# Kernel optimization log

Measured on AMD Instinct MI355X. Metric: run time of the kernel, lower is better.

## Reference

```python
import jax, jax.numpy as jnp
import numpy as np

B, S, L, V = 512, 17, 81, 13030
ENC, OE, PE, H = 240, 80, 60, 200
IN = ENC + OE + PE  # 380
TEMPERATURE = 1.0


def setup_inputs() -> dict:
    key = jax.random.key(0)
    ks = jax.random.split(key, 16)
    enc = jax.random.normal(ks[0], (B, L, ENC), dtype=jnp.float32)
    in_adj_phase = jnp.zeros((B,), dtype=bool)
    loc_idxs = jax.random.randint(ks[1], (B, L), 0, S)  # which step each location decodes at
    order_masks = jax.random.bernoulli(ks[2], 0.2, (B, S, V))
    power_1h = jnp.eye(7, dtype=jnp.float32)[jax.random.randint(ks[3], (B,), 0, 7)]
    w = 0.1
    return {
        'enc': enc,
        'in_adj_phase': in_adj_phase,
        'loc_idxs': loc_idxs,
        'order_masks': order_masks,
        'power_1h': power_1h,
        'order_embedding': w * jax.random.normal(ks[4], (V, OE), dtype=jnp.float32),
        'power_W': w * jax.random.normal(ks[5], (PE, 7), dtype=jnp.float32),
        'power_b': w * jax.random.normal(ks[6], (PE,), dtype=jnp.float32),
        'W_ih': w * jax.random.normal(ks[7], (4 * H, IN), dtype=jnp.float32),
        'W_hh': w * jax.random.normal(ks[8], (4 * H, H), dtype=jnp.float32),
        'b_ih': w * jax.random.normal(ks[9], (4 * H,), dtype=jnp.float32),
        'b_hh': w * jax.random.normal(ks[10], (4 * H,), dtype=jnp.float32),
        'out_W': w * jax.random.normal(ks[11], (V, H), dtype=jnp.float32),
        'out_b': w * jax.random.normal(ks[12], (V,), dtype=jnp.float32),
        'master_alignments': jax.random.uniform(ks[13], (L, L), dtype=jnp.float32),
    }


def reference(enc, in_adj_phase, loc_idxs, order_masks, power_1h,
              order_embedding, power_W, power_b, W_ih, W_hh, b_ih, b_hh,
              out_W, out_b, master_alignments):
    # eval mode: dropout masks are not applied (self.training is False)
    power_emb = power_1h @ power_W.T + power_b  # [B, PE]
    invalid = ~jnp.any(loc_idxs != -1, axis=1)  # [B] rows with no orders to give
    keys = jax.random.split(jax.random.key(42), S)

    def step_fn(carry, xs):
        h, c, order_emb = carry
        step, mask_t, k = xs  # mask_t: [B, V]
        # alignment over locations decoded at this step
        sel = ((loc_idxs == step) | (loc_idxs == -2)).astype(enc.dtype)  # [B, L]
        align = sel @ master_alignments  # [B, L]
        denom = jnp.sum(align, axis=1, keepdims=True)
        align = jnp.where(denom != 0, align / denom, 0.0)  # NaN -> 0 as in torch
        loc_enc = jnp.einsum('bl,bld->bd', align, enc)  # [B, ENC]
        x = jnp.concatenate([loc_enc, order_emb, power_emb], axis=1)  # [B, IN]
        gates = x @ W_ih.T + b_ih + h @ W_hh.T + b_hh  # torch gate order i,f,g,o
        i, f, g, o = jnp.split(gates, 4, axis=1)
        c_new = jax.nn.sigmoid(f) * c + jax.nn.sigmoid(i) * jnp.tanh(g)
        h_new = jax.nn.sigmoid(o) * jnp.tanh(c_new)
        scores = h_new @ out_W.T + out_b  # [B, V]
        m = jnp.where(invalid[:, None], True, mask_t)
        scores = jnp.minimum(scores, m.astype(scores.dtype) * 1e9 - 1e8)
        idx = jax.random.categorical(k, scores / TEMPERATURE, axis=-1)  # [B]
        order_emb_new = order_embedding[idx]  # [B, OE]
        return (h_new, c_new, order_emb_new), (idx, scores)

    carry0 = (jnp.zeros((B, H), enc.dtype), jnp.zeros((B, H), enc.dtype),
              jnp.zeros((B, OE), enc.dtype))
    xs = (jnp.arange(S), jnp.transpose(order_masks, (1, 0, 2)), keys)
    _, (idxs, scores) = jax.lax.scan(step_fn, carry0, xs)
    return jnp.transpose(idxs, (1, 0)), jnp.transpose(scores, (1, 0, 2))
```

## Files before the change

kernel.cpp:

```cpp
#include <hip/hip_runtime.h>
#include <math.h>

#define NB 512
#define NS 17
#define NL 81
#define NV 13030
#define NENC 240
#define NOE 80
#define NPE 60
#define NH 200
#define NIN 380
#define NG 800
#define KP 224
#define KG 608
#define NVP 13056
#define NGP 832
#define NBLK 204

#define XH_ENC 224
#define XH_OE  464
#define XH_PE  544

typedef short bf8_t __attribute__((ext_vector_type(8)));
typedef float f4_t __attribute__((ext_vector_type(4)));

__device__ __forceinline__ unsigned short f2bf(float f) {
  unsigned u = __float_as_uint(f);
  unsigned r = (u + 0x7fffu + ((u >> 16) & 1u)) >> 16;
  return (unsigned short)r;
}

__device__ __host__ __forceinline__ unsigned rotl32h(unsigned x, int d) {
  return (x << d) | (x >> (32 - d));
}
__device__ __host__ __forceinline__ void threefry2x32(
    unsigned k0, unsigned k1, unsigned x0, unsigned x1,
    unsigned& y0, unsigned& y1) {
  unsigned ks2 = k0 ^ k1 ^ 0x1BD11BDAu;
  x0 += k0; x1 += k1;
#define TFR(r) { x0 += x1; x1 = rotl32h(x1, r); x1 ^= x0; }
  TFR(13) TFR(15) TFR(26) TFR(6)
  x0 += k1;  x1 += ks2 + 1u;
  TFR(17) TFR(29) TFR(16) TFR(24)
  x0 += ks2; x1 += k0 + 2u;
  TFR(13) TFR(15) TFR(26) TFR(6)
  x0 += k0;  x1 += k1 + 3u;
  TFR(17) TFR(29) TFR(16) TFR(24)
  x0 += k1;  x1 += ks2 + 4u;
  TFR(13) TFR(15) TFR(26) TFR(6)
  x0 += ks2; x1 += k0 + 5u;
#undef TFR
  y0 = x0; y1 = x1;
}

__device__ __forceinline__ float gumbel_from_bits(unsigned bits) {
  float u = __uint_as_float((bits >> 9) | 0x3f800000u) - 1.0f;
  if (u == 0.0f) u = 1.17549435e-38f;
  return -__logf(-__logf(u));
}

__global__ void __launch_bounds__(256) prep_wcat_kernel(
    const float* __restrict__ W_ih, const float* __restrict__ W_hh,
    unsigned short* __restrict__ Wcat) {
  int t = blockIdx.x * 256 + threadIdx.x;
  if (t >= NGP * KG) return;
  int n = t / KG, k = t % KG;
  float v = 0.f;
  if (n < NG) {
    if (k < NH) v = W_hh[n * NH + k];
    else if (k >= XH_ENC && k < XH_PE + NPE) v = W_ih[n * NIN + (k - XH_ENC)];
  }
  Wcat[t] = f2bf(v);
}

__global__ void __launch_bounds__(256) prep_outw_kernel(
    const float* __restrict__ out_W, unsigned short* __restrict__ outWb) {
  int t = blockIdx.x * 256 + threadIdx.x;
  if (t >= NVP * KP) return;
  int n = t / KP, k = t % KP;
  outWb[t] = f2bf((n < NV && k < NH) ? out_W[n * NH + k] : 0.f);
}

__global__ void __launch_bounds__(256) misc_kernel(
    const float* __restrict__ power_1h, const float* __restrict__ power_W,
    const float* __restrict__ power_b, const int* __restrict__ loc_idxs,
    const float* __restrict__ b_ih, const float* __restrict__ b_hh,
    unsigned short* __restrict__ xh, float* __restrict__ bcat,
    int* __restrict__ invalid) {
  int t = blockIdx.x * 256 + threadIdx.x;
  if (t < NB * NPE) {
    int b = t / NPE, p = t % NPE;
    float a = power_b[p];
#pragma unroll
    for (int k = 0; k < 7; ++k) a = fmaf(power_1h[b * 7 + k], power_W[p * 7 + k], a);
    xh[(size_t)b * KG + XH_PE + p] = f2bf(a);
  }
  if (t < NG) bcat[t] = b_ih[t] + b_hh[t];
  if (t < NB) {
    bool any = false;
    for (int l = 0; l < NL; ++l) any = any || (loc_idxs[t * NL + l] != -1);
    invalid[t] = any ? 0 : 1;
  }
}

__global__ void __launch_bounds__(256) build_x_kernel(
    const int* __restrict__ loc_idxs, const float* __restrict__ MA,
    const float* __restrict__ enc, unsigned short* __restrict__ xh, int step) {
  __shared__ float sel[NL];
  __shared__ float aln[NL];
  __shared__ float denom;
  const int b = blockIdx.x, tid = threadIdx.x;
  if (tid < NL) {
    int li = loc_idxs[b * NL + tid];
    sel[tid] = (li == step || li == -2) ? 1.0f : 0.0f;
  }
  __syncthreads();
  if (tid < NL) {
    float a = 0.f;
    for (int l = 0; l < NL; ++l) a = fmaf(sel[l], MA[l * NL + tid], a);
    aln[tid] = a;
  }
  __syncthreads();
  if (tid == 0) {
    float d = 0.f;
    for (int l = 0; l < NL; ++l) d += aln[l];
    denom = d;
  }
  __syncthreads();
  if (tid < NL) aln[tid] = (denom != 0.f) ? aln[tid] / denom : 0.0f;
  __syncthreads();
  if (tid < NENC) {
    const float* eb = enc + (size_t)b * NL * NENC + tid;
    float a = 0.f;
    for (int l = 0; l < NL; ++l) a = fmaf(aln[l], eb[(size_t)l * NENC], a);
    xh[(size_t)b * KG + XH_ENC + tid] = f2bf(a);
  }
}

__device__ __forceinline__ void mfma_nt_16x64(
    const unsigned short* __restrict__ A, const unsigned short* __restrict__ B,
    int lda, int ldb, int m0w, int n0, int nk, f4_t acc[4]) {
  const int lane = threadIdx.x & 63;
  const int tx = lane & 15, quad = lane >> 4;
  const unsigned short* ap = A + (size_t)(m0w + tx) * lda + quad * 8;
  const unsigned short* bp0 = B + (size_t)(n0 + tx) * ldb + quad * 8;
  for (int kc = 0; kc < nk; ++kc) {
    bf8_t a = *(const bf8_t*)(ap + kc * 32);
#pragma unroll
    for (int jf = 0; jf < 4; ++jf) {
      bf8_t b = *(const bf8_t*)(bp0 + (size_t)jf * 16 * ldb + kc * 32);
      acc[jf] = __builtin_amdgcn_mfma_f32_16x16x32_bf16(a, b, acc[jf], 0, 0, 0);
    }
  }
}

__global__ void __launch_bounds__(256) gates_kernel(
    const unsigned short* __restrict__ xh, const unsigned short* __restrict__ Wcat,
    const float* __restrict__ bcat, float* __restrict__ gates) {
  const int w = threadIdx.x >> 6;
  const int lane = threadIdx.x & 63;
  const int tx = lane & 15, quad = lane >> 4;
  const int m0w = blockIdx.y * 64 + w * 16;
  const int n0 = blockIdx.x * 64;
  f4_t acc[4] = {};
  mfma_nt_16x64(xh, Wcat, KG, KG, m0w, n0, KG / 32, acc);
#pragma unroll
  for (int jf = 0; jf < 4; ++jf) {
    int n = n0 + jf * 16 + tx;
    if (n >= NG) continue;
    float bias = bcat[n];
#pragma unroll
    for (int reg = 0; reg < 4; ++reg) {
      int m = m0w + quad * 4 + reg;
      gates[(size_t)m * NG + n] = acc[jf][reg] + bias;
    }
  }
}

__global__ void __launch_bounds__(256) lstm_cell_kernel(
    const float* __restrict__ gates, unsigned short* __restrict__ xh,
    float* __restrict__ c) {
  int t = blockIdx.x * 256 + threadIdx.x;
  if (t >= NB * NH) return;
  int b = t / NH, j = t % NH;
  const float* g = gates + (size_t)b * NG;
  float gi = g[j], gf = g[NH + j], gg = g[2 * NH + j], go = g[3 * NH + j];
  float si = 1.f / (1.f + expf(-gi));
  float sf = 1.f / (1.f + expf(-gf));
  float so = 1.f / (1.f + expf(-go));
  float cn = sf * c[t] + si * tanhf(gg);
  float hn = so * tanhf(cn);
  c[t] = cn;
  xh[(size_t)b * KG + j] = f2bf(hn);
}

__global__ void __launch_bounds__(256) scores_kernel(
    const unsigned short* __restrict__ xh, const unsigned short* __restrict__ outWb,
    const float* __restrict__ out_b, const int* __restrict__ order_masks,
    const int* __restrict__ invalid, float* __restrict__ out,
    float* __restrict__ pval, int* __restrict__ pidx,
    int step, unsigned k0, unsigned k1) {
  const int w = threadIdx.x >> 6;
  const int lane = threadIdx.x & 63;
  const int tx = lane & 15, quad = lane >> 4;
  const int m0w = blockIdx.y * 64 + w * 16;
  const int n0 = blockIdx.x * 64;
  f4_t acc[4] = {};
  mfma_nt_16x64(xh, outWb, KG, KP, m0w, n0, KP / 32, acc);

  float bias[4];
  int nn[4];
#pragma unroll
  for (int jf = 0; jf < 4; ++jf) {
    nn[jf] = n0 + jf * 16 + tx;
    bias[jf] = (nn[jf] < NV) ? out_b[nn[jf]] : 0.f;
  }

  float bval[4];
  int bidx[4];
#pragma unroll
  for (int reg = 0; reg < 4; ++reg) {
    const int m = m0w + quad * 4 + reg;
    const int inv = invalid[m];
    const int* mrow = order_masks + (size_t)m * NS * NV + (size_t)step * NV;
    float* orow = out + (size_t)NB * NS + ((size_t)m * NS + step) * (size_t)NV;
    float vals[4];
#pragma unroll
    for (int jf = 0; jf < 4; ++jf) {
      int n = nn[jf];
      float v = -1.0e8f;
      if (n < NV) {
        int msk = inv ? 1 : mrow[n];
        v = fminf(acc[jf][reg] + bias[jf], msk ? 9.0e8f : -1.0e8f);
        orow[n] = v;
      }
      vals[jf] = v;
    }
    unsigned base = (unsigned)m * (unsigned)NV;
    unsigned y0, y1, y2, y3;
    threefry2x32(k0, k1, base + (unsigned)nn[0], base + (unsigned)nn[1], y0, y1);
    threefry2x32(k0, k1, base + (unsigned)nn[2], base + (unsigned)nn[3], y2, y3);
    float g[4] = {gumbel_from_bits(y0), gumbel_from_bits(y1),
                  gumbel_from_bits(y2), gumbel_from_bits(y3)};
    float bv = -INFINITY; int bi = 0;
#pragma unroll
    for (int jf = 0; jf < 4; ++jf) {
      float cnd = (nn[jf] < NV) ? vals[jf] + g[jf] : -INFINITY;
      if (cnd > bv) { bv = cnd; bi = nn[jf]; }
    }
    bval[reg] = bv; bidx[reg] = bi;
  }
#pragma unroll
  for (int s = 8; s >= 1; s >>= 1) {
#pragma unroll
    for (int reg = 0; reg < 4; ++reg) {
      float ov = __shfl_xor(bval[reg], s);
      int oi = __shfl_xor(bidx[reg], s);
      if (ov > bval[reg]) { bval[reg] = ov; bidx[reg] = oi; }
    }
  }
#pragma unroll
  for (int reg = 0; reg < 4; ++reg) {
    if (tx == reg) {
      int m = m0w + quad * 4 + reg;
      pval[(size_t)m * NBLK + blockIdx.x] = bval[reg];
      pidx[(size_t)m * NBLK + blockIdx.x] = bidx[reg];
    }
  }
}

__global__ void __launch_bounds__(256) sample_kernel(
    const float* __restrict__ pval, const int* __restrict__ pidx,
    const float* __restrict__ order_embedding, unsigned short* __restrict__ xh,
    float* __restrict__ out, int step) {
  const int m = blockIdx.x, tid = threadIdx.x;
  __shared__ float sv[256];
  __shared__ int si[256];
  float v = -INFINITY; int i = 0;
  if (tid < NBLK) { v = pval[(size_t)m * NBLK + tid]; i = pidx[(size_t)m * NBLK + tid]; }
  sv[tid] = v; si[tid] = i;
  __syncthreads();
  for (int off = 128; off > 0; off >>= 1) {
    if (tid < off) {
      float v2 = sv[tid + off]; int i2 = si[tid + off];
      if (v2 > sv[tid] || (v2 == sv[tid] && i2 < si[tid])) { sv[tid] = v2; si[tid] = i2; }
    }
    __syncthreads();
  }
  if (tid == 0) out[m * NS + step] = (float)si[0];
  if (tid < NOE) {
    int idx = si[0];
    xh[(size_t)m * KG + XH_OE + tid] = f2bf(order_embedding[(size_t)idx * NOE + tid]);
  }
}

extern "C" void kernel_launch(void* const* d_in, const int* in_sizes, int n_in,
                              void* d_out, int out_size, void* d_ws, size_t ws_size,
                              hipStream_t stream) {
  const float* enc          = (const float*)d_in[0];
  const int*   loc_idxs     = (const int*)d_in[2];
  const int*   order_masks  = (const int*)d_in[3];
  const float* power_1h     = (const float*)d_in[4];
  const float* order_embedding = (const float*)d_in[5];
  const float* power_W      = (const float*)d_in[6];
  const float* power_b      = (const float*)d_in[7];
  const float* W_ih         = (const float*)d_in[8];
  const float* W_hh         = (const float*)d_in[9];
  const float* b_ih         = (const float*)d_in[10];
  const float* b_hh         = (const float*)d_in[11];
  const float* out_W        = (const float*)d_in[12];
  const float* out_b        = (const float*)d_in[13];
  const float* MA           = (const float*)d_in[14];

  float* ws      = (float*)d_ws;
  float* c       = ws;
  float* gates   = c + NB * NH;
  float* pval    = gates + NB * NG;
  float* bcat    = pval + NB * NBLK;
  int*   pidx    = (int*)(bcat + NG);
  int*   invalid = pidx + NB * NBLK;
  unsigned short* xh    = (unsigned short*)(invalid + NB);
  unsigned short* Wcat  = xh + (size_t)NB * KG;
  unsigned short* outWb = Wcat + (size_t)NGP * KG;

  float* out = (float*)d_out;

  hipMemsetAsync(xh, 0, sizeof(unsigned short) * (size_t)NB * KG, stream);
  hipMemsetAsync(c, 0, sizeof(float) * (size_t)NB * NH, stream);
  misc_kernel<<<(NB * NPE + 255) / 256, 256, 0, stream>>>(
      power_1h, power_W, power_b, loc_idxs, b_ih, b_hh, xh, bcat, invalid);
  prep_wcat_kernel<<<(NGP * KG + 255) / 256, 256, 0, stream>>>(W_ih, W_hh, Wcat);
  prep_outw_kernel<<<(NVP * KP + 255) / 256, 256, 0, stream>>>(out_W, outWb);

  unsigned key[2 * NS];
  for (unsigned i = 0; i < NS; ++i) {
    unsigned y0, y1;
    threefry2x32(0u, 42u, i, i + NS, y0, y1);
    key[2 * i] = y0;
    threefry2x32(0u, 42u, i, i + NS, y0, y1);
    key[2 * i + 1] = y1;
  }

  dim3 gGates(NGP / 64, NB / 64);
  dim3 gScores(NBLK, NB / 64);
  for (int s = 0; s < NS; ++s) {
    build_x_kernel<<<NB, 256, 0, stream>>>(loc_idxs, MA, enc, xh, s);
    gates_kernel<<<gGates, 256, 0, stream>>>(xh, Wcat, bcat, gates);
    lstm_cell_kernel<<<(NB * NH + 255) / 256, 256, 0, stream>>>(gates, xh, c);
    scores_kernel<<<gScores, 256, 0, stream>>>(
        xh, outWb, out_b, order_masks, invalid, out, pval, pidx,
        s, key[2 * s], key[2 * s + 1]);
    sample_kernel<<<NB, 256, 0, stream>>>(pval, pidx, order_embedding, xh, out, s);
  }
}
```

Before: 1.942 ms.

## Hoist input projections out of LSTM loop and fuse gates, cell and sampling

The parts of the input-gate projection that do not depend on the recurrence are precomputed once before the loop. These are the location-encoding contribution for every step, the power embedding plus bias, and a table of order-embedding gate contributions over the whole vocabulary. Each step then only does the h·W_hh GEMM, fused with the LSTM cell, the previous step's argmax reduction and a table lookup. This cuts per-step launches and GEMM width, in exchange for larger precomputed buffers. The precomputed gate terms are stored in bf16, which adds rounding, and the argmax tie-break is made deterministic.

```diff
diff --git a/kernel.cpp b/kernel.cpp
--- a/kernel.cpp
+++ b/kernel.cpp
@@ -12,14 +12,12 @@
 #define NIN 380
 #define NG 800
 #define KP 224
-#define KG 608
+#define KE 256
+#define KO 96
 #define NVP 13056
 #define NGP 832
 #define NBLK 204
-
-#define XH_ENC 224
-#define XH_OE  464
-#define XH_PE  544
+#define LDG 840
 
 typedef short bf8_t __attribute__((ext_vector_type(8)));
 typedef float f4_t __attribute__((ext_vector_type(4)));
@@ -28,6 +26,9 @@
   unsigned u = __float_as_uint(f);
   unsigned r = (u + 0x7fffu + ((u >> 16) & 1u)) >> 16;
   return (unsigned short)r;
+}
+__device__ __forceinline__ float bf2f(unsigned short u) {
+  return __uint_as_float((unsigned)u << 16);
 }
 
 __device__ __host__ __forceinline__ unsigned rotl32h(unsigned x, int d) {
@@ -59,84 +60,6 @@
   return -__logf(-__logf(u));
 }
 
-__global__ void __launch_bounds__(256) prep_wcat_kernel(
-    const float* __restrict__ W_ih, const float* __restrict__ W_hh,
-    unsigned short* __restrict__ Wcat) {
-  int t = blockIdx.x * 256 + threadIdx.x;
-  if (t >= NGP * KG) return;
-  int n = t / KG, k = t % KG;
-  float v = 0.f;
-  if (n < NG) {
-    if (k < NH) v = W_hh[n * NH + k];
-    else if (k >= XH_ENC && k < XH_PE + NPE) v = W_ih[n * NIN + (k - XH_ENC)];
-  }
-  Wcat[t] = f2bf(v);
-}
-
-__global__ void __launch_bounds__(256) prep_outw_kernel(
-    const float* __restrict__ out_W, unsigned short* __restrict__ outWb) {
-  int t = blockIdx.x * 256 + threadIdx.x;
-  if (t >= NVP * KP) return;
-  int n = t / KP, k = t % KP;
-  outWb[t] = f2bf((n < NV && k < NH) ? out_W[n * NH + k] : 0.f);
-}
-
-__global__ void __launch_bounds__(256) misc_kernel(
-    const float* __restrict__ power_1h, const float* __restrict__ power_W,
-    const float* __restrict__ power_b, const int* __restrict__ loc_idxs,
-    const float* __restrict__ b_ih, const float* __restrict__ b_hh,
-    unsigned short* __restrict__ xh, float* __restrict__ bcat,
-    int* __restrict__ invalid) {
-  int t = blockIdx.x * 256 + threadIdx.x;
-  if (t < NB * NPE) {
-    int b = t / NPE, p = t % NPE;
-    float a = power_b[p];
-#pragma unroll
-    for (int k = 0; k < 7; ++k) a = fmaf(power_1h[b * 7 + k], power_W[p * 7 + k], a);
-    xh[(size_t)b * KG + XH_PE + p] = f2bf(a);
-  }
-  if (t < NG) bcat[t] = b_ih[t] + b_hh[t];
-  if (t < NB) {
-    bool any = false;
-    for (int l = 0; l < NL; ++l) any = any || (loc_idxs[t * NL + l] != -1);
-    invalid[t] = any ? 0 : 1;
-  }
-}
-
-__global__ void __launch_bounds__(256) build_x_kernel(
-    const int* __restrict__ loc_idxs, const float* __restrict__ MA,
-    const float* __restrict__ enc, unsigned short* __restrict__ xh, int step) {
-  __shared__ float sel[NL];
-  __shared__ float aln[NL];
-  __shared__ float denom;
-  const int b = blockIdx.x, tid = threadIdx.x;
-  if (tid < NL) {
-    int li = loc_idxs[b * NL + tid];
-    sel[tid] = (li == step || li == -2) ? 1.0f : 0.0f;
-  }
-  __syncthreads();
-  if (tid < NL) {
-    float a = 0.f;
-    for (int l = 0; l < NL; ++l) a = fmaf(sel[l], MA[l * NL + tid], a);
-    aln[tid] = a;
-  }
-  __syncthreads();
-  if (tid == 0) {
-    float d = 0.f;
-    for (int l = 0; l < NL; ++l) d += aln[l];
-    denom = d;
-  }
-  __syncthreads();
-  if (tid < NL) aln[tid] = (denom != 0.f) ? aln[tid] / denom : 0.0f;
-  __syncthreads();
-  if (tid < NENC) {
-    const float* eb = enc + (size_t)b * NL * NENC + tid;
-    float a = 0.f;
-    for (int l = 0; l < NL; ++l) a = fmaf(aln[l], eb[(size_t)l * NENC], a);
-    xh[(size_t)b * KG + XH_ENC + tid] = f2bf(a);
-  }
-}
-
 __device__ __forceinline__ void mfma_nt_16x64(
     const unsigned short* __restrict__ A, const unsigned short* __restrict__ B,
     int lda, int ldb, int m0w, int n0, int nk, f4_t acc[4]) {
@@ -154,44 +77,239 @@
   }
 }
 
-__global__ void __launch_bounds__(256) gates_kernel(
-    const unsigned short* __restrict__ xh, const unsigned short* __restrict__ Wcat,
-    const float* __restrict__ bcat, float* __restrict__ gates) {
+#define PK_WHH  (NGP * KP)
+#define PK_WIHE (NGP * KE)
+#define PK_WIHO (NGP * KO)
+#define PK_OEB  (NVP * KO)
+#define PK_OUTW (NVP * KP)
+#define PK_TOT  (PK_WHH + PK_WIHE + PK_WIHO + PK_OEB + PK_OUTW)
+
+__global__ void __launch_bounds__(256) pack_kernel(
+    const float* __restrict__ W_hh, const float* __restrict__ W_ih,
+    const float* __restrict__ order_embedding, const float* __restrict__ out_W,
+    unsigned short* __restrict__ Whh_b, unsigned short* __restrict__ WihEb,
+    unsigned short* __restrict__ WihOb, unsigned short* __restrict__ oeb,
+    unsigned short* __restrict__ outWb) {
+  int t = blockIdx.x * 256 + threadIdx.x;
+  if (t >= PK_TOT) return;
+  if (t < PK_WHH) {
+    int n = t / KP, k = t % KP;
+    Whh_b[t] = f2bf((n < NG && k < NH) ? W_hh[n * NH + k] : 0.f);
+    return;
+  }
+  t -= PK_WHH;
+  if (t < PK_WIHE) {
+    int n = t / KE, k = t % KE;
+    WihEb[t] = f2bf((n < NG && k < NENC) ? W_ih[n * NIN + k] : 0.f);
+    return;
+  }
+  t -= PK_WIHE;
+  if (t < PK_WIHO) {
+    int n = t / KO, k = t % KO;
+    WihOb[t] = f2bf((n < NG && k < NOE) ? W_ih[n * NIN + NENC + k] : 0.f);
+    return;
+  }
+  t -= PK_WIHO;
+  if (t < PK_OEB) {
+    int v = t / KO, k = t % KO;
+    oeb[t] = f2bf((v < NV && k < NOE) ? order_embedding[v * NOE + k] : 0.f);
+    return;
+  }
+  t -= PK_OEB;
+  {
+    int v = t / KP, k = t % KP;
+    outWb[t] = f2bf((v < NV && k < NH) ? out_W[v * NH + k] : 0.f);
+  }
+}
+
+__global__ void __launch_bounds__(256) misc_kernel(
+    const float* __restrict__ power_1h, const float* __restrict__ power_W,
+    const float* __restrict__ power_b, const int* __restrict__ loc_idxs,
+    float* __restrict__ power_emb, int* __restrict__ invalid) {
+  int t = blockIdx.x * 256 + threadIdx.x;
+  if (t < NB * NPE) {
+    int b = t / NPE, p = t % NPE;
+    float a = power_b[p];
+#pragma unroll
+    for (int k = 0; k < 7; ++k) a = fmaf(power_1h[b * 7 + k], power_W[p * 7 + k], a);
+    power_emb[t] = a;
+  }
+  if (t < NB) {
+    bool any = false;
+    for (int l = 0; l < NL; ++l) any = any || (loc_idxs[t * NL + l] != -1);
+    invalid[t] = any ? 0 : 1;
+  }
+}
+
+__global__ void __launch_bounds__(256) gpow_kernel(
+    const float* __restrict__ power_emb, const float* __restrict__ W_ih,
+    const float* __restrict__ b_ih, const float* __restrict__ b_hh,
+    float* __restrict__ gpow) {
+  int t = blockIdx.x * 256 + threadIdx.x;
+  if (t >= NB * NGP) return;
+  int b = t / NGP, n = t % NGP;
+  float v = 0.f;
+  if (n < NG) {
+    v = b_ih[n] + b_hh[n];
+    const float* pe = power_emb + b * NPE;
+    const float* wp = W_ih + (size_t)n * NIN + NENC + NOE;
+    for (int p = 0; p < NPE; ++p) v = fmaf(pe[p], wp[p], v);
+  }
+  gpow[t] = v;
+}
+
+__global__ void __launch_bounds__(256) lenc_kernel(
+    const int* __restrict__ loc_idxs, const float* __restrict__ MA,
+    const float* __restrict__ enc, unsigned short* __restrict__ lencb) {
+  __shared__ float encs[NL * NENC];
+  __shared__ float sel[NL];
+  __shared__ float aln[NL];
+  __shared__ float denom;
+  const int b = blockIdx.x, tid = threadIdx.x;
+  for (int i = tid; i < NL * NENC; i += 256) encs[i] = enc[(size_t)b * NL * NENC + i];
+  int myloc = (tid < NL) ? loc_idxs[b * NL + tid] : 0;
+  __syncthreads();
+  for (int s = 0; s < NS; ++s) {
+    if (tid < NL) sel[tid] = (myloc == s || myloc == -2) ? 1.0f : 0.0f;
+    __syncthreads();
+    if (tid < NL) {
+      float a = 0.f;
+      for (int l = 0; l < NL; ++l) a = fmaf(sel[l], MA[l * NL + tid], a);
+      aln[tid] = a;
+    }
+    __syncthreads();
+    if (tid == 0) {
+      float d = 0.f;
+      for (int l = 0; l < NL; ++l) d += aln[l];
+      denom = d;
+    }
+    __syncthreads();
+    if (tid < NL) aln[tid] = (denom != 0.f) ? aln[tid] / denom : 0.0f;
+    __syncthreads();
+    unsigned short* orow = lencb + ((size_t)b * NS + s) * KE;
+    if (tid < KE) {
+      float a = 0.f;
+      if (tid < NENC) {
+        for (int l = 0; l < NL; ++l) a = fmaf(aln[l], encs[l * NENC + tid], a);
+      }
+      orow[tid] = f2bf(a);
+    }
+    __syncthreads();
+  }
+}
+
+__global__ void __launch_bounds__(256) gstat_kernel(
+    const unsigned short* __restrict__ lencb, const unsigned short* __restrict__ WihEb,
+    const float* __restrict__ gpow, unsigned short* __restrict__ gstat) {
   const int w = threadIdx.x >> 6;
   const int lane = threadIdx.x & 63;
   const int tx = lane & 15, quad = lane >> 4;
   const int m0w = blockIdx.y * 64 + w * 16;
   const int n0 = blockIdx.x * 64;
   f4_t acc[4] = {};
-  mfma_nt_16x64(xh, Wcat, KG, KG, m0w, n0, KG / 32, acc);
+  mfma_nt_16x64(lencb, WihEb, KE, KE, m0w, n0, KE / 32, acc);
 #pragma unroll
   for (int jf = 0; jf < 4; ++jf) {
     int n = n0 + jf * 16 + tx;
-    if (n >= NG) continue;
-    float bias = bcat[n];
 #pragma unroll
     for (int reg = 0; reg < 4; ++reg) {
       int m = m0w + quad * 4 + reg;
-      gates[(size_t)m * NG + n] = acc[jf][reg] + bias;
-    }
-  }
-}
-
-__global__ void __launch_bounds__(256) lstm_cell_kernel(
-    const float* __restrict__ gates, unsigned short* __restrict__ xh,
-    float* __restrict__ c) {
-  int t = blockIdx.x * 256 + threadIdx.x;
-  if (t >= NB * NH) return;
-  int b = t / NH, j = t % NH;
-  const float* g = gates + (size_t)b * NG;
-  float gi = g[j], gf = g[NH + j], gg = g[2 * NH + j], go = g[3 * NH + j];
-  float si = 1.f / (1.f + expf(-gi));
-  float sf = 1.f / (1.f + expf(-gf));
-  float so = 1.f / (1.f + expf(-go));
-  float cn = sf * c[t] + si * tanhf(gg);
-  float hn = so * tanhf(cn);
-  c[t] = cn;
-  xh[(size_t)b * KG + j] = f2bf(hn);
+      int b = m / NS;
+      gstat[(size_t)m * NGP + n] = f2bf(acc[jf][reg] + gpow[(size_t)b * NGP + n]);
+    }
+  }
+}
+
+__global__ void __launch_bounds__(256) oeg_kernel(
+    const unsigned short* __restrict__ oeb, const unsigned short* __restrict__ WihOb,
+    unsigned short* __restrict__ OEG) {
+  const int w = threadIdx.x >> 6;
+  const int lane = threadIdx.x & 63;
+  const int tx = lane & 15, quad = lane >> 4;
+  const int m0w = blockIdx.y * 64 + w * 16;
+  const int n0 = blockIdx.x * 64;
+  f4_t acc[4] = {};
+  mfma_nt_16x64(oeb, WihOb, KO, KO, m0w, n0, KO / 32, acc);
+#pragma unroll
+  for (int jf = 0; jf < 4; ++jf) {
+    int n = n0 + jf * 16 + tx;
+#pragma unroll
+    for (int reg = 0; reg < 4; ++reg) {
+      int m = m0w + quad * 4 + reg;
+      OEG[(size_t)m * NGP + n] = f2bf(acc[jf][reg]);
+    }
+  }
+}
+
+__global__ void __launch_bounds__(256) gates_cell_kernel(
+    unsigned short* __restrict__ xh, const unsigned short* __restrict__ Whh_b,
+    const unsigned short* __restrict__ gstat, const unsigned short* __restrict__ OEG,
+    const float* __restrict__ pval, const int* __restrict__ pidx,
+    float* __restrict__ c, float* __restrict__ out, int step) {
+  __shared__ float gs[16 * LDG];
+  __shared__ int sidx[16];
+  const int m0 = blockIdx.x * 16;
+  const int tid = threadIdx.x;
+  if (step > 0) {
+    int r = tid >> 4, sub = tid & 15;
+    float bv = -INFINITY; int bi = 0x7fffffff;
+    for (int t = sub; t < NBLK; t += 16) {
+      float v = pval[(size_t)(m0 + r) * NBLK + t];
+      int i = pidx[(size_t)(m0 + r) * NBLK + t];
+      if (v > bv || (v == bv && i < bi)) { bv = v; bi = i; }
+    }
+#pragma unroll
+    for (int s = 8; s >= 1; s >>= 1) {
+      float ov = __shfl_xor(bv, s);
+      int oi = __shfl_xor(bi, s);
+      if (ov > bv || (ov == bv && oi < bi)) { bv = ov; bi = oi; }
+    }
+    if (sub == 0) {
+      sidx[r] = bi;
+      out[(m0 + r) * NS + step - 1] = (float)bi;
+    }
+  } else {
+    if (tid < 16) sidx[tid] = NV;
+  }
+  __syncthreads();
+  const int w = tid >> 6;
+  const int lane = tid & 63;
+  const int tx = lane & 15, quad = lane >> 4;
+  for (int jt = w; jt < NGP / 64; jt += 4) {
+    f4_t acc[4] = {};
+    mfma_nt_16x64(xh, Whh_b, KP, KP, m0, jt * 64, KP / 32, acc);
+#pragma unroll
+    for (int jf = 0; jf < 4; ++jf) {
+      int n = jt * 64 + jf * 16 + tx;
+#pragma unroll
+      for (int reg = 0; reg < 4; ++reg)
+        gs[(quad * 4 + reg) * LDG + n] = acc[jf][reg];
+    }
+  }
+  __syncthreads();
+  for (int e = tid; e < 16 * NH; e += 256) {
+    int r = e / NH, j = e - r * NH;
+    int m = m0 + r;
+    const float* L = gs + r * LDG;
+    size_t gr = ((size_t)m * NS + step) * NGP;
+    size_t er = (size_t)sidx[r] * NGP;
+    float gi = L[j]          + bf2f(gstat[gr + j])          + bf2f(OEG[er + j]);
+    float gf = L[NH + j]     + bf2f(gstat[gr + NH + j])     + bf2f(OEG[er + NH + j]);
+    float gg = L[2 * NH + j] + bf2f(gstat[gr + 2 * NH + j]) + bf2f(OEG[er + 2 * NH + j]);
+    float go = L[3 * NH + j] + bf2f(gstat[gr + 3 * NH + j]) + bf2f(OEG[er + 3 * NH + j]);
+    float si = 1.f / (1.f + __expf(-gi));
+    float sf = 1.f / (1.f + __expf(-gf));
+    float so = 1.f / (1.f + __expf(-go));
+    float tg = fminf(fmaxf(gg, -15.f), 15.f);
+    float e2 = __expf(2.f * tg);
+    float th = (e2 - 1.f) / (e2 + 1.f);
+    float cn = sf * c[(size_t)m * NH + j] + si * th;
+    float tc = fminf(fmaxf(cn, -15.f), 15.f);
+    float ec = __expf(2.f * tc);
+    float hn = so * (ec - 1.f) / (ec + 1.f);
+    c[(size_t)m * NH + j] = cn;
+    xh[(size_t)m * KP + j] = f2bf(hn);
+  }
 }
 
 __global__ void __launch_bounds__(256) scores_kernel(
@@ -206,7 +324,7 @@
   const int m0w = blockIdx.y * 64 + w * 16;
   const int n0 = blockIdx.x * 64;
   f4_t acc[4] = {};
-  mfma_nt_16x64(xh, outWb, KG, KP, m0w, n0, KP / 32, acc);
+  mfma_nt_16x64(xh, outWb, KP, KP, m0w, n0, KP / 32, acc);
 
   float bias[4];
   int nn[4];
@@ -256,7 +374,9 @@
     for (int reg = 0; reg < 4; ++reg) {
       float ov = __shfl_xor(bval[reg], s);
       int oi = __shfl_xor(bidx[reg], s);
-      if (ov > bval[reg]) { bval[reg] = ov; bidx[reg] = oi; }
+      if (ov > bval[reg] || (ov == bval[reg] && oi < bidx[reg])) {
+        bval[reg] = ov; bidx[reg] = oi;
+      }
     }
   }
 #pragma unroll
@@ -269,29 +389,25 @@
   }
 }
 
-__global__ void __launch_bounds__(256) sample_kernel(
+__global__ void __launch_bounds__(256) final_idx_kernel(
     const float* __restrict__ pval, const int* __restrict__ pidx,
-    const float* __restrict__ order_embedding, unsigned short* __restrict__ xh,
-    float* __restrict__ out, int step) {
-  const int m = blockIdx.x, tid = threadIdx.x;
-  __shared__ float sv[256];
-  __shared__ int si[256];
-  float v = -INFINITY; int i = 0;
-  if (tid < NBLK) { v = pval[(size_t)m * NBLK + tid]; i = pidx[(size_t)m * NBLK + tid]; }
-  sv[tid] = v; si[tid] = i;
-  __syncthreads();
-  for (int off = 128; off > 0; off >>= 1) {
-    if (tid < off) {
-      float v2 = sv[tid + off]; int i2 = si[tid + off];
-      if (v2 > sv[tid] || (v2 == sv[tid] && i2 < si[tid])) { sv[tid] = v2; si[tid] = i2; }
-    }
-    __syncthreads();
-  }
-  if (tid == 0) out[m * NS + step] = (float)si[0];
-  if (tid < NOE) {
-    int idx = si[0];
-    xh[(size_t)m * KG + XH_OE + tid] = f2bf(order_embedding[(size_t)idx * NOE + tid]);
-  }
+    float* __restrict__ out) {
+  const int m0 = blockIdx.x * 16;
+  const int tid = threadIdx.x;
+  int r = tid >> 4, sub = tid & 15;
+  float bv = -INFINITY; int bi = 0x7fffffff;
+  for (int t = sub; t < NBLK; t += 16) {
+    float v = pval[(size_t)(m0 + r) * NBLK + t];
+    int i = pidx[(size_t)(m0 + r) * NBLK + t];
+    if (v > bv || (v == bv && i < bi)) { bv = v; bi = i; }
+  }
+#pragma unroll
+  for (int s = 8; s >= 1; s >>= 1) {
+    float ov = __shfl_xor(bv, s);
+    int oi = __shfl_xor(bi, s);
+    if (ov > bv || (ov == bv && oi < bi)) { bv = ov; bi = oi; }
+  }
+  if (sub == 0) out[(m0 + r) * NS + NS - 1] = (float)bi;
 }
 
 extern "C" void kernel_launch(void* const* d_in, const int* in_sizes, int n_in,
@@ -312,44 +428,54 @@
   const float* out_b        = (const float*)d_in[13];
   const float* MA           = (const float*)d_in[14];
 
-  float* ws      = (float*)d_ws;
-  float* c       = ws;
-  float* gates   = c + NB * NH;
-  float* pval    = gates + NB * NG;
-  float* bcat    = pval + NB * NBLK;
-  int*   pidx    = (int*)(bcat + NG);
-  int*   invalid = pidx + NB * NBLK;
-  unsigned short* xh    = (unsigned short*)(invalid + NB);
-  unsigned short* Wcat  = xh + (size_t)NB * KG;
-  unsigned short* outWb = Wcat + (size_t)NGP * KG;
+  char* p = (char*)d_ws;
+  float* c         = (float*)p;            p += (size_t)NB * NH * 4;
+  float* pval      = (float*)p;            p += (size_t)NB * NBLK * 4;
+  int*   pidx      = (int*)p;              p += (size_t)NB * NBLK * 4;
+  int*   invalid   = (int*)p;              p += (size_t)NB * 4;
+  float* power_emb = (float*)p;            p += (size_t)NB * NPE * 4;
+  float* gpow      = (float*)p;            p += (size_t)NB * NGP * 4;
+  unsigned short* xh    = (unsigned short*)p; p += (size_t)NB * KP * 2;
+  unsigned short* Whh_b = (unsigned short*)p; p += (size_t)NGP * KP * 2;
+  unsigned short* WihEb = (unsigned short*)p; p += (size_t)NGP * KE * 2;
+  unsigned short* WihOb = (unsigned short*)p; p += (size_t)NGP * KO * 2;
+  unsigned short* oeb   = (unsigned short*)p; p += (size_t)NVP * KO * 2;
+  unsigned short* outWb = (unsigned short*)p; p += (size_t)NVP * KP * 2;
+  unsigned short* lencb = (unsigned short*)p; p += (size_t)NB * NS * KE * 2;
+  unsigned short* gstat = (unsigned short*)p; p += (size_t)NB * NS * NGP * 2;
+  unsigned short* OEG   = (unsigned short*)p; p += (size_t)NVP * NGP * 2;
 
   float* out = (float*)d_out;
 
-  hipMemsetAsync(xh, 0, sizeof(unsigned short) * (size_t)NB * KG, stream);
+  hipMemsetAsync(xh, 0, sizeof(unsigned short) * (size_t)NB * KP, stream);
   hipMemsetAsync(c, 0, sizeof(float) * (size_t)NB * NH, stream);
+
+  pack_kernel<<<(PK_TOT + 255) / 256, 256, 0, stream>>>(
+      W_hh, W_ih, order_embedding, out_W, Whh_b, WihEb, WihOb, oeb, outWb);
   misc_kernel<<<(NB * NPE + 255) / 256, 256, 0, stream>>>(
-      power_1h, power_W, power_b, loc_idxs, b_ih, b_hh, xh, bcat, invalid);
-  prep_wcat_kernel<<<(NGP * KG + 255) / 256, 256, 0, stream>>>(W_ih, W_hh, Wcat);
-  prep_outw_kernel<<<(NVP * KP + 255) / 256, 256, 0, stream>>>(out_W, outWb);
+      power_1h, power_W, power_b, loc_idxs, power_emb, invalid);
+  gpow_kernel<<<(NB * NGP + 255) / 256, 256, 0, stream>>>(
+      power_emb, W_ih, b_ih, b_hh, gpow);
+  lenc_kernel<<<NB, 256, 0, stream>>>(loc_idxs, MA, enc, lencb);
+  gstat_kernel<<<dim3(NGP / 64, NB * NS / 64), 256, 0, stream>>>(
+      lencb, WihEb, gpow, gstat);
+  oeg_kernel<<<dim3(NGP / 64, NVP / 64), 256, 0, stream>>>(oeb, WihOb, OEG);
 
   unsigned key[2 * NS];
   for (unsigned i = 0; i < NS; ++i) {
     unsigned y0, y1;
     threefry2x32(0u, 42u, i, i + NS, y0, y1);
     key[2 * i] = y0;
-    threefry2x32(0u, 42u, i, i + NS, y0, y1);
     key[2 * i + 1] = y1;
   }
 
-  dim3 gGates(NGP / 64, NB / 64);
   dim3 gScores(NBLK, NB / 64);
   for (int s = 0; s < NS; ++s) {
-    build_x_kernel<<<NB, 256, 0, stream>>>(loc_idxs, MA, enc, xh, s);
-    gates_kernel<<<gGates, 256, 0, stream>>>(xh, Wcat, bcat, gates);
-    lstm_cell_kernel<<<(NB * NH + 255) / 256, 256, 0, stream>>>(gates, xh, c);
+    gates_cell_kernel<<<NB / 16, 256, 0, stream>>>(
+        xh, Whh_b, gstat, OEG, pval, pidx, c, out, s);
     scores_kernel<<<gScores, 256, 0, stream>>>(
         xh, outWb, out_b, order_masks, invalid, out, pval, pidx,
         s, key[2 * s], key[2 * s + 1]);
-    sample_kernel<<<NB, 256, 0, stream>>>(pval, pidx, order_embedding, xh, out, s);
-  }
-}
+  }
+  final_idx_kernel<<<NB / 16, 256, 0, stream>>>(pval, pidx, out);
+}
```

New measurement: 2.212 ms. 1.14x slower.
